# Optimization experiments

Hardware: AMD Instinct MI355X
Metric: run time of the kernel (lower is better)

Reference implementation:

```python
import math
import jax, jax.numpy as jnp
import numpy as np

GRID = (256, 256, 256)
K = 9                # kernel_size (already odd)
SIGMA = K / 4.0
PAD = K // 2
CLIP = 0.03


def _gaussian_kernel():
    ax = np.arange(K, dtype=np.float32)
    mean = (K - 1) / 2.0
    g = np.exp(-(((ax - mean) / SIGMA) ** 2) / 2.0) / (SIGMA * math.sqrt(2.0 * math.pi))
    k = g[:, None, None] * g[None, :, None] * g[None, None, :]
    k = k / k.sum()
    return jnp.asarray(k, dtype=jnp.float32).reshape(1, 1, K, K, K)  # OIDHW


def setup_inputs() -> dict:
    key = jax.random.key(0)
    x = jax.random.normal(key, (int(np.prod(GRID)),), dtype=jnp.float32)
    kernel = _gaussian_kernel()
    return {"x": x, "kernel": kernel}


def reference(x, kernel):
    v = x.reshape(1, 1, *GRID)  # [1,1,D,H,W]
    # reflect padding (torch padding_mode='reflect', padding = K//2)
    p = jnp.pad(v, ((0, 0), (0, 0), (PAD, PAD), (PAD, PAD), (PAD, PAD)), mode="reflect")
    # torch Conv3d is cross-correlation; lax conv does not flip kernels either
    out = jax.lax.conv_general_dilated(
        p, kernel,
        window_strides=(1, 1, 1),
        padding="VALID",
        dimension_numbers=("NCDHW", "OIDHW", "NCDHW"),
    )
    # clip: keep smoothed output within +/-CLIP of the original input
    out = jnp.maximum(jnp.minimum(v, out + CLIP), out - CLIP)
    return out.reshape(-1)
```

## Files before the change

### kernel.cpp

```cpp
#include <hip/hip_runtime.h>
#include <hip/hip_fp16.h>
#include <math.h>

#define CLIPV 0.03f

struct W9 { float g[9]; };
struct half4 { __half2 a, b; };

__device__ __forceinline__ int reflect_idx(int i, int n) {
    if (i < 0) i = -i;
    if (i >= n) i = 2 * n - 2 - i;
    return i;
}

__device__ __forceinline__ float4 h4_to_f4(half4 v) {
    const float2 ab = __half22float2(v.a), cd = __half22float2(v.b);
    float4 r; r.x = ab.x; r.y = ab.y; r.z = cd.x; r.w = cd.y; return r;
}
__device__ __forceinline__ half4 f4_to_h4(float4 v) {
    half4 r; r.a = __floats2half2_rn(v.x, v.y); r.b = __floats2half2_rn(v.z, v.w);
    return r;
}

__global__ __launch_bounds__(256) void w_pass(const float* __restrict__ x,
                                              __half* __restrict__ t1, W9 wt) {
    const int bid = blockIdx.x;
    const int xcd = bid & 7;
    const int k   = bid >> 3;
    const int z   = xcd * 32 + (k >> 3);
    const int wv  = threadIdx.x >> 6;
    const int h0  = (k & 7) * 32 + wv * 8;
    const int L   = threadIdx.x & 63;
    const int w4  = L * 4;
    const bool l0 = (L == 0), l63 = (L == 63);
    const int offL = l0 ? 1 : (w4 - 4);
    const int offR = l63 ? 251 : (w4 + 4);

    const float* plane  = x  + (size_t)z * 65536;
    __half*      oplane = t1 + (size_t)z * 65536;

    float4 cL, cC, cR;
    {
        const float* row = plane + (size_t)h0 * 256;
        cL = *(const float4*)(row + offL);
        cC = *(const float4*)(row + w4);
        cR = *(const float4*)(row + offR);
    }

    #pragma unroll
    for (int i = 0; i < 8; ++i) {
        float4 nL, nC, nR;
        if (i < 7) {
            const float* row = plane + (size_t)(h0 + i + 1) * 256;
            nL = *(const float4*)(row + offL);
            nC = *(const float4*)(row + w4);
            nR = *(const float4*)(row + offR);
        }

        float sv[12];
        sv[0] = l0 ? cL.w : cL.x;
        sv[1] = l0 ? cL.z : cL.y;
        sv[2] = l0 ? cL.y : cL.z;
        sv[3] = l0 ? cL.x : cL.w;
        sv[4] = cC.x; sv[5] = cC.y; sv[6] = cC.z; sv[7] = cC.w;
        sv[8]  = l63 ? cR.w : cR.x;
        sv[9]  = l63 ? cR.z : cR.y;
        sv[10] = l63 ? cR.y : cR.z;
        sv[11] = l63 ? cR.x : cR.w;

        float4 wc;
        {
            float a0 = 0.f, a1 = 0.f, a2 = 0.f, a3 = 0.f;
            #pragma unroll
            for (int j = 0; j < 9; ++j) {
                a0 = fmaf(wt.g[j], sv[j],     a0);
                a1 = fmaf(wt.g[j], sv[j + 1], a1);
                a2 = fmaf(wt.g[j], sv[j + 2], a2);
                a3 = fmaf(wt.g[j], sv[j + 3], a3);
            }
            wc.x = a0; wc.y = a1; wc.z = a2; wc.w = a3;
        }
        *(half4*)(oplane + (size_t)(h0 + i) * 256 + w4) = f4_to_h4(wc);

        cL = nL; cC = nC; cR = nR;
    }
}

__global__ __launch_bounds__(256) void h2_pass(const __half* __restrict__ t1,
                                               __half* __restrict__ t2, W9 wt) {
    const int bid = blockIdx.x;
    const int xcd = bid & 7;
    const int k   = bid >> 3;
    const int z   = xcd * 32 + (k >> 3);
    const int wv  = threadIdx.x >> 6;
    const int h0  = (k & 7) * 32 + wv * 8;
    const int w4  = (threadIdx.x & 63) * 4;

    const __half* plane  = t1 + (size_t)z * 65536;
    __half*       oplane = t2 + (size_t)z * 65536;

    float4 ring[9];

    half4 cur = *(const half4*)(plane + (size_t)reflect_idx(h0 - 4, 256) * 256 + w4);
    half4 nxt = *(const half4*)(plane + (size_t)reflect_idx(h0 - 3, 256) * 256 + w4);

    #pragma unroll
    for (int i = 0; i < 16; ++i) {
        half4 nn;
        if (i < 14)
            nn = *(const half4*)(plane + (size_t)reflect_idx(h0 - 2 + i, 256) * 256 + w4);

        ring[i % 9] = h4_to_f4(cur);

        if (i >= 8) {
            float a0 = 0.f, a1 = 0.f, a2 = 0.f, a3 = 0.f;
            #pragma unroll
            for (int j = 0; j < 9; ++j) {
                const float4 v = ring[(i - 8 + j) % 9];
                a0 = fmaf(wt.g[j], v.x, a0);
                a1 = fmaf(wt.g[j], v.y, a1);
                a2 = fmaf(wt.g[j], v.z, a2);
                a3 = fmaf(wt.g[j], v.w, a3);
            }
            float4 o; o.x = a0; o.y = a1; o.z = a2; o.w = a3;
            *(half4*)(oplane + (size_t)(h0 + i - 8) * 256 + w4) = f4_to_h4(o);
        }

        cur = nxt; nxt = nn;
    }
}

__global__ __launch_bounds__(256) void d_clip_pass(const __half* __restrict__ t2,
                                                   const float* __restrict__ x,
                                                   float* __restrict__ out, W9 wt) {
    const int bid   = blockIdx.x;
    const int xcd   = bid & 7;
    const int k     = bid >> 3;
    const int chunk = xcd * 4 + (k & 3);
    const int tile  = k >> 2;
    const int z0    = chunk * 8;
    const size_t c4 = (size_t)tile * 256 + threadIdx.x;

    const half4*  t4 = (const half4*)t2;
    const float4* xp = (const float4*)x;
    float4*       o4 = (float4*)out;

    float4 ring[9];

    half4 cur = t4[(size_t)reflect_idx(z0 - 4, 256) * 16384 + c4];
    half4 nxt = t4[(size_t)reflect_idx(z0 - 3, 256) * 16384 + c4];
    float4 cX, nX;

    #pragma unroll
    for (int i = 0; i < 16; ++i) {
        half4 nn;
        if (i < 14)
            nn = t4[(size_t)reflect_idx(z0 - 2 + i, 256) * 16384 + c4];
        if (i >= 7 && i < 15)
            nX = xp[(size_t)(z0 + i - 7) * 16384 + c4];

        ring[i % 9] = h4_to_f4(cur);

        if (i >= 8) {
            const int z = z0 + i - 8;
            float a0 = 0.f, a1 = 0.f, a2 = 0.f, a3 = 0.f;
            #pragma unroll
            for (int j = 0; j < 9; ++j) {
                const float4 v = ring[(i - 8 + j) % 9];
                a0 = fmaf(wt.g[j], v.x, a0);
                a1 = fmaf(wt.g[j], v.y, a1);
                a2 = fmaf(wt.g[j], v.z, a2);
                a3 = fmaf(wt.g[j], v.w, a3);
            }
            float4 r;
            r.x = fmaxf(fminf(cX.x, a0 + CLIPV), a0 - CLIPV);
            r.y = fmaxf(fminf(cX.y, a1 + CLIPV), a1 - CLIPV);
            r.z = fmaxf(fminf(cX.z, a2 + CLIPV), a2 - CLIPV);
            r.w = fmaxf(fminf(cX.w, a3 + CLIPV), a3 - CLIPV);
            o4[(size_t)z * 16384 + c4] = r;
        }

        cur = nxt; nxt = nn;
        cX = nX;
    }
}

extern "C" void kernel_launch(void* const* d_in, const int* in_sizes, int n_in,
                              void* d_out, int out_size, void* d_ws, size_t ws_size,
                              hipStream_t stream) {
    const float* x = (const float*)d_in[0];
    float* out = (float*)d_out;
    __half* t1 = (__half*)d_ws;
    __half* t2 = t1 + 16777216;

    W9 wt;
    {
        double g[9], s = 0.0;
        const double sigma = 9.0 / 4.0;
        for (int i = 0; i < 9; ++i) {
            double tt = (i - 4.0) / sigma;
            g[i] = exp(-0.5 * tt * tt);
            s += g[i];
        }
        for (int i = 0; i < 9; ++i) wt.g[i] = (float)(g[i] / s);
    }

    w_pass<<<dim3(2048), dim3(256), 0, stream>>>(x, t1, wt);
    h2_pass<<<dim3(2048), dim3(256), 0, stream>>>(t1, t2, wt);
    d_clip_pass<<<dim3(2048), dim3(256), 0, stream>>>(t2, x, out, wt);
}
```

Baseline: 56.98 us.

## Double per-thread work, deepen prefetch, and use nontemporal loads/stores in clip pass

Each of the three separable passes now has every wave cover 16 rows or depth slices instead of 8, and the grid is halved. The longer strip cuts the redundant 8-row halo reads in the H and D passes. The W pass prefetches two rows ahead with a 3-slot register ring. The D/clip pass uses nontemporal loads for x and nontemporal stores for the output to keep those streams from polluting cache. Occupancy hints are added via launch_bounds, at the cost of more registers and fewer blocks to balance across CUs.

Result: slower. 74.05 us (+30.0%).

```diff
diff --git a/kernel.cpp b/kernel.cpp
--- a/kernel.cpp
+++ b/kernel.cpp
@@ -6,6 +6,7 @@
 
 struct W9 { float g[9]; };
 struct half4 { __half2 a, b; };
+typedef float nt4 __attribute__((ext_vector_type(4)));
 
 __device__ __forceinline__ int reflect_idx(int i, int n) {
     if (i < 0) i = -i;
@@ -22,14 +23,14 @@
     return r;
 }
 
-__global__ __launch_bounds__(256) void w_pass(const float* __restrict__ x,
-                                              __half* __restrict__ t1, W9 wt) {
+__global__ __launch_bounds__(256, 4) void w_pass(const float* __restrict__ x,
+                                                 __half* __restrict__ t1, W9 wt) {
     const int bid = blockIdx.x;
     const int xcd = bid & 7;
     const int k   = bid >> 3;
-    const int z   = xcd * 32 + (k >> 3);
+    const int z   = xcd * 32 + (k >> 2);
     const int wv  = threadIdx.x >> 6;
-    const int h0  = (k & 7) * 32 + wv * 8;
+    const int h0  = ((k & 3) * 4 + wv) * 16;
     const int L   = threadIdx.x & 63;
     const int w4  = L * 4;
     const bool l0 = (L == 0), l63 = (L == 63);
@@ -39,23 +40,27 @@
     const float* plane  = x  + (size_t)z * 65536;
     __half*      oplane = t1 + (size_t)z * 65536;
 
-    float4 cL, cC, cR;
+    float4 sL[3], sC[3], sR[3];
     {
         const float* row = plane + (size_t)h0 * 256;
-        cL = *(const float4*)(row + offL);
-        cC = *(const float4*)(row + w4);
-        cR = *(const float4*)(row + offR);
+        sL[0] = *(const float4*)(row + offL);
+        sC[0] = *(const float4*)(row + w4);
+        sR[0] = *(const float4*)(row + offR);
+        row += 256;
+        sL[1] = *(const float4*)(row + offL);
+        sC[1] = *(const float4*)(row + w4);
+        sR[1] = *(const float4*)(row + offR);
     }
 
     #pragma unroll
-    for (int i = 0; i < 8; ++i) {
-        float4 nL, nC, nR;
-        if (i < 7) {
-            const float* row = plane + (size_t)(h0 + i + 1) * 256;
-            nL = *(const float4*)(row + offL);
-            nC = *(const float4*)(row + w4);
-            nR = *(const float4*)(row + offR);
-        }
+    for (int i = 0; i < 16; ++i) {
+        if (i < 14) {
+            const float* row = plane + (size_t)(h0 + i + 2) * 256;
+            sL[(i + 2) % 3] = *(const float4*)(row + offL);
+            sC[(i + 2) % 3] = *(const float4*)(row + w4);
+            sR[(i + 2) % 3] = *(const float4*)(row + offR);
+        }
+        const float4 cL = sL[i % 3], cC = sC[i % 3], cR = sR[i % 3];
 
         float sv[12];
         sv[0] = l0 ? cL.w : cL.x;
@@ -81,19 +86,17 @@
             wc.x = a0; wc.y = a1; wc.z = a2; wc.w = a3;
         }
         *(half4*)(oplane + (size_t)(h0 + i) * 256 + w4) = f4_to_h4(wc);
-
-        cL = nL; cC = nC; cR = nR;
-    }
-}
-
-__global__ __launch_bounds__(256) void h2_pass(const __half* __restrict__ t1,
-                                               __half* __restrict__ t2, W9 wt) {
+    }
+}
+
+__global__ __launch_bounds__(256, 4) void h2_pass(const __half* __restrict__ t1,
+                                                  __half* __restrict__ t2, W9 wt) {
     const int bid = blockIdx.x;
     const int xcd = bid & 7;
     const int k   = bid >> 3;
-    const int z   = xcd * 32 + (k >> 3);
+    const int z   = xcd * 32 + (k >> 2);
     const int wv  = threadIdx.x >> 6;
-    const int h0  = (k & 7) * 32 + wv * 8;
+    const int h0  = ((k & 3) * 4 + wv) * 16;
     const int w4  = (threadIdx.x & 63) * 4;
 
     const __half* plane  = t1 + (size_t)z * 65536;
@@ -105,9 +108,9 @@
     half4 nxt = *(const half4*)(plane + (size_t)reflect_idx(h0 - 3, 256) * 256 + w4);
 
     #pragma unroll
-    for (int i = 0; i < 16; ++i) {
+    for (int i = 0; i < 24; ++i) {
         half4 nn;
-        if (i < 14)
+        if (i < 22)
             nn = *(const half4*)(plane + (size_t)reflect_idx(h0 - 2 + i, 256) * 256 + w4);
 
         ring[i % 9] = h4_to_f4(cur);
@@ -130,34 +133,36 @@
     }
 }
 
-__global__ __launch_bounds__(256) void d_clip_pass(const __half* __restrict__ t2,
-                                                   const float* __restrict__ x,
-                                                   float* __restrict__ out, W9 wt) {
+__global__ __launch_bounds__(256, 4) void d_clip_pass(const __half* __restrict__ t2,
+                                                      const float* __restrict__ x,
+                                                      float* __restrict__ out, W9 wt) {
     const int bid   = blockIdx.x;
     const int xcd   = bid & 7;
     const int k     = bid >> 3;
-    const int chunk = xcd * 4 + (k & 3);
-    const int tile  = k >> 2;
-    const int z0    = chunk * 8;
+    const int chunk = xcd * 2 + (k & 1);
+    const int tile  = k >> 1;
+    const int z0    = chunk * 16;
     const size_t c4 = (size_t)tile * 256 + threadIdx.x;
 
-    const half4*  t4 = (const half4*)t2;
-    const float4* xp = (const float4*)x;
-    float4*       o4 = (float4*)out;
+    const half4* t4 = (const half4*)t2;
+    const nt4*   xp = (const nt4*)x;
+    nt4*         o4 = (nt4*)out;
 
     float4 ring[9];
+    nt4 xs[2];
 
     half4 cur = t4[(size_t)reflect_idx(z0 - 4, 256) * 16384 + c4];
     half4 nxt = t4[(size_t)reflect_idx(z0 - 3, 256) * 16384 + c4];
-    float4 cX, nX;
 
     #pragma unroll
-    for (int i = 0; i < 16; ++i) {
+    for (int i = 0; i < 24; ++i) {
+        const nt4 xv = xs[i % 2];
+
         half4 nn;
-        if (i < 14)
+        if (i < 22)
             nn = t4[(size_t)reflect_idx(z0 - 2 + i, 256) * 16384 + c4];
-        if (i >= 7 && i < 15)
-            nX = xp[(size_t)(z0 + i - 7) * 16384 + c4];
+        if (i >= 6 && i < 22)
+            xs[i % 2] = __builtin_nontemporal_load(&xp[(size_t)(z0 + i - 6) * 16384 + c4]);
 
         ring[i % 9] = h4_to_f4(cur);
 
@@ -172,16 +177,15 @@
                 a2 = fmaf(wt.g[j], v.z, a2);
                 a3 = fmaf(wt.g[j], v.w, a3);
             }
-            float4 r;
-            r.x = fmaxf(fminf(cX.x, a0 + CLIPV), a0 - CLIPV);
-            r.y = fmaxf(fminf(cX.y, a1 + CLIPV), a1 - CLIPV);
-            r.z = fmaxf(fminf(cX.z, a2 + CLIPV), a2 - CLIPV);
-            r.w = fmaxf(fminf(cX.w, a3 + CLIPV), a3 - CLIPV);
-            o4[(size_t)z * 16384 + c4] = r;
+            nt4 r;
+            r.x = fmaxf(fminf(xv.x, a0 + CLIPV), a0 - CLIPV);
+            r.y = fmaxf(fminf(xv.y, a1 + CLIPV), a1 - CLIPV);
+            r.z = fmaxf(fminf(xv.z, a2 + CLIPV), a2 - CLIPV);
+            r.w = fmaxf(fminf(xv.w, a3 + CLIPV), a3 - CLIPV);
+            __builtin_nontemporal_store(r, &o4[(size_t)z * 16384 + c4]);
         }
 
         cur = nxt; nxt = nn;
-        cX = nX;
     }
 }
 
@@ -205,7 +209,7 @@
         for (int i = 0; i < 9; ++i) wt.g[i] = (float)(g[i] / s);
     }
 
-    w_pass<<<dim3(2048), dim3(256), 0, stream>>>(x, t1, wt);
-    h2_pass<<<dim3(2048), dim3(256), 0, stream>>>(t1, t2, wt);
-    d_clip_pass<<<dim3(2048), dim3(256), 0, stream>>>(t2, x, out, wt);
-}
+    w_pass<<<dim3(1024), dim3(256), 0, stream>>>(x, t1, wt);
+    h2_pass<<<dim3(1024), dim3(256), 0, stream>>>(t1, t2, wt);
+    d_clip_pass<<<dim3(1024), dim3(256), 0, stream>>>(t2, x, out, wt);
+}
```
